# Kernel tuning notes

Measured on AMD Instinct MI355X. Metric: run time of the kernel, lower is better.

Reference implementation:

```python
import jax, jax.numpy as jnp
import numpy as np

HIDDEN = 2048
HEADS = 16
HEAD_DIM = HIDDEN // HEADS


def setup_inputs() -> dict:
    key = jax.random.key(0)
    ks = jax.random.split(key, 9)
    s = 0.02
    return {
        "hidden_state": jax.random.normal(ks[0], (2, 2048, HIDDEN), dtype=jnp.float32),
        "Wq": jax.random.normal(ks[1], (HIDDEN, HIDDEN), dtype=jnp.float32) * s,
        "bq": jnp.zeros((HIDDEN,), dtype=jnp.float32),
        "Wk": jax.random.normal(ks[2], (HIDDEN, HIDDEN), dtype=jnp.float32) * s,
        "bk": jnp.zeros((HIDDEN,), dtype=jnp.float32),
        "Wv": jax.random.normal(ks[3], (HIDDEN, HIDDEN), dtype=jnp.float32) * s,
        "bv": jnp.zeros((HIDDEN,), dtype=jnp.float32),
        "Wo": jax.random.normal(ks[4], (HIDDEN, HIDDEN), dtype=jnp.float32) * s,
        "bo": jnp.zeros((HIDDEN,), dtype=jnp.float32),
    }


def _split_head(x):
    b, s, _ = x.shape
    return x.reshape(b, s, HEADS, HEAD_DIM).transpose(0, 2, 1, 3)  # [B,H,S,D]


def reference(hidden_state, Wq, bq, Wk, bk, Wv, bv, Wo, bo):
    scale = 1.0 / (HEAD_DIM ** 0.5)
    # nn.Linear: x @ W.T + b
    q = _split_head(hidden_state @ Wq.T + bq)
    k = _split_head(hidden_state @ Wk.T + bk)
    v = _split_head(hidden_state @ Wv.T + bv)
    scores = jnp.einsum("bhqd,bhkd->bhqk", q, k) * scale  # [B,H,S,S]
    probs = jax.nn.softmax(scores, axis=-1)
    # dropout treated as identity (eval mode)
    out = jnp.einsum("bhqk,bhkd->bhqd", probs, v)  # [B,H,S,D]
    b, h, s, d = out.shape
    out = out.transpose(0, 2, 1, 3).reshape(b, s, h * d)
    return out @ Wo.T + bo
```

## Files before the change

### kernel.cpp

```cpp
#include <hip/hip_runtime.h>
#include <hip/hip_bf16.h>


typedef __attribute__((ext_vector_type(8))) short bf16x8;
typedef __attribute__((ext_vector_type(4))) float f32x4;
typedef unsigned short ushort_t;

#define MFMA_16x16x32(a, b, c) __builtin_amdgcn_mfma_f32_16x16x32_bf16((a), (b), (c), 0, 0, 0)

__device__ __forceinline__ ushort_t f2bf(float f) {
  unsigned int u = __builtin_bit_cast(unsigned int, f);
  u += 0x7fffu + ((u >> 16) & 1u);
  return (ushort_t)(u >> 16);
}

__device__ __forceinline__ void gload_lds16(const void* g, void* lds) {
  __builtin_amdgcn_global_load_lds(
      (const __attribute__((address_space(1))) unsigned int*)g,
      (__attribute__((address_space(3))) unsigned int*)(unsigned int)(unsigned long long)lds,
      16, 0, 0);
}

__global__ __launch_bounds__(256) void f2bf_kernel(const float* __restrict__ in,
                                                   ushort_t* __restrict__ out, int n4) {
  int i = blockIdx.x * blockDim.x + threadIdx.x;
  const int stride = gridDim.x * blockDim.x;
  for (; i < n4; i += stride) {
    const float4 v = ((const float4*)in)[i];
    ushort4 o;
    o.x = f2bf(v.x); o.y = f2bf(v.y); o.z = f2bf(v.z); o.w = f2bf(v.w);
    ((ushort4*)out)[i] = o;
  }
}

template <int MODE>
__global__ __launch_bounds__(256) void gemm_bt_kernel(const ushort_t* __restrict__ A,
                                                      const ushort_t* __restrict__ B,
                                                      const float* __restrict__ bias,
                                                      void* __restrict__ Cout,
                                                      int M, int N, int K) {
  __shared__ __align__(16) char smem[16384];
  char* sA = smem;
  char* sB = smem + 8192;
  const int tid = threadIdx.x;
  const int wave = tid >> 6;
  const int lane = tid & 63;
  const int wr = wave >> 1, wc = wave & 1;
  const int brow = blockIdx.y * 128;
  const int bcol = blockIdx.x * 128;

  const f32x4 fzero = {0.f, 0.f, 0.f, 0.f};
  f32x4 acc[4][4];
#pragma unroll
  for (int i = 0; i < 4; ++i)
#pragma unroll
    for (int j = 0; j < 4; ++j) acc[i][j] = fzero;

  const int srow = lane >> 2;
  const int koff = (lane & 3) * 8;

  for (int kt = 0; kt < K; kt += 32) {
#pragma unroll
    for (int c = 0; c < 2; ++c) {
      const int ch = wave + c * 4;
      gload_lds16(A + (size_t)(brow + ch * 16 + srow) * K + kt + koff, sA + ch * 1024);
      gload_lds16(B + (size_t)(bcol + ch * 16 + srow) * K + kt + koff, sB + ch * 1024);
    }
    __syncthreads();
    bf16x8 af[4], bfr[4];
#pragma unroll
    for (int i = 0; i < 4; ++i)
      af[i] = *(const bf16x8*)(sA + (wr * 64 + i * 16 + (lane & 15)) * 64 + (lane >> 4) * 16);
#pragma unroll
    for (int j = 0; j < 4; ++j)
      bfr[j] = *(const bf16x8*)(sB + (wc * 64 + j * 16 + (lane & 15)) * 64 + (lane >> 4) * 16);
#pragma unroll
    for (int i = 0; i < 4; ++i)
#pragma unroll
      for (int j = 0; j < 4; ++j) acc[i][j] = MFMA_16x16x32(af[i], bfr[j], acc[i][j]);
    __syncthreads();
  }

#pragma unroll
  for (int i = 0; i < 4; ++i) {
#pragma unroll
    for (int j = 0; j < 4; ++j) {
#pragma unroll
      for (int r = 0; r < 4; ++r) {
        const int row = brow + wr * 64 + i * 16 + (lane >> 4) * 4 + r;
        const int col = bcol + wc * 64 + j * 16 + (lane & 15);
        const float v = acc[i][j][r] + ((MODE == 2) ? bias[row] : bias[col]);
        if (MODE == 0) {
          ((float*)Cout)[(size_t)row * N + col] = v;
        } else if (MODE == 1) {
          const int b = row >> 11, s = row & 2047;
          const int h = col >> 7, d = col & 127;
          ((ushort_t*)Cout)[(((size_t)b * 16 + h) * 2048 + s) * 128 + d] = f2bf(v);
        } else {
          const int h = row >> 7, d = row & 127;
          const int b = col >> 11, s = col & 2047;
          ((ushort_t*)Cout)[(((size_t)b * 16 + h) * 128 + d) * 2048 + s] = f2bf(v);
        }
      }
    }
  }
}

__global__ __launch_bounds__(256) void attn_kernel(const ushort_t* __restrict__ Q,
                                                   const ushort_t* __restrict__ K,
                                                   const ushort_t* __restrict__ Vt,
                                                   ushort_t* __restrict__ O) {
  constexpr int S = 2048, D = 128, H = 16;
  __shared__ __align__(16) char smem[16384 + 16384 + 9216];
  char* sK = smem;
  char* sVt = smem + 16384;
  char* sP = smem + 32768;

  const int tid = threadIdx.x;
  const int wave = tid >> 6;
  const int lane = tid & 63;
  const int g = lane >> 4;
  const int l15 = lane & 15;
  const int qt = blockIdx.x & 31;
  const int bh = blockIdx.x >> 5;
  const int b = bh >> 4, h = bh & 15;

  const ushort_t* Qb = Q + (size_t)bh * S * D;
  const char* Kb = (const char*)(K + (size_t)bh * S * D);
  const char* Vtb = (const char*)(Vt + (size_t)bh * D * S);
  const int q0 = qt * 64 + wave * 16;

  bf16x8 aq[4];
  {
    const ushort_t* qrow = Qb + (size_t)(q0 + l15) * D + g * 8;
#pragma unroll
    for (int kk = 0; kk < 4; ++kk) aq[kk] = *(const bf16x8*)(qrow + kk * 32);
  }

  const char* kg[4];
  const char* vg[4];
#pragma unroll
  for (int i = 0; i < 4; ++i) {
    const int po = (wave * 4 + i) * 1024 + lane * 16;
    const int lk = po ^ (((po >> 8) & 7) << 4);
    kg[i] = Kb + (size_t)(lk >> 8) * 256 + (lk & 255);
    const int lv = po ^ (((po >> 7) & 7) << 4);
    vg[i] = Vtb + (size_t)(lv >> 7) * 4096 + (lv & 127);
  }

  const f32x4 fzero = {0.f, 0.f, 0.f, 0.f};
  f32x4 o[8];
#pragma unroll
  for (int nt = 0; nt < 8; ++nt) o[nt] = fzero;
  float row_m[4] = {-1e30f, -1e30f, -1e30f, -1e30f};
  float row_l[4] = {0.f, 0.f, 0.f, 0.f};

  char* sPw = sP + wave * 2304;
  const float scale = 0.08838834764831845f;
  const float LOG2E = 1.4426950408889634f;

  for (int kv0 = 0; kv0 < S; kv0 += 64) {
    __syncthreads();
#pragma unroll
    for (int i = 0; i < 4; ++i)
      gload_lds16(kg[i] + (size_t)kv0 * 256, sK + (wave * 4 + i) * 1024);
#pragma unroll
    for (int i = 0; i < 4; ++i)
      gload_lds16(vg[i] + (size_t)kv0 * 2, sVt + (wave * 4 + i) * 1024);
    __syncthreads();

    f32x4 sfrag[4];
#pragma unroll
    for (int nt = 0; nt < 4; ++nt) {
      sfrag[nt] = fzero;
#pragma unroll
      for (int kk = 0; kk < 4; ++kk) {
        const int row = nt * 16 + l15;
        const int la = row * 256 + kk * 64 + g * 16;
        const bf16x8 bk = *(const bf16x8*)(sK + (la ^ ((row & 7) << 4)));
        sfrag[nt] = MFMA_16x16x32(aq[kk], bk, sfrag[nt]);
      }
    }

#pragma unroll
    for (int r = 0; r < 4; ++r) {
      const float s0 = sfrag[0][r] * scale;
      const float s1 = sfrag[1][r] * scale;
      const float s2 = sfrag[2][r] * scale;
      const float s3 = sfrag[3][r] * scale;
      float mx = fmaxf(fmaxf(s0, s1), fmaxf(s2, s3));
      mx = fmaxf(mx, __shfl_xor(mx, 1));
      mx = fmaxf(mx, __shfl_xor(mx, 2));
      mx = fmaxf(mx, __shfl_xor(mx, 4));
      mx = fmaxf(mx, __shfl_xor(mx, 8));
      if (!__all(mx - row_m[r] <= 8.0f)) {
        const float nm = fmaxf(row_m[r], mx);
        const float corr = exp2f((row_m[r] - nm) * LOG2E);
        row_l[r] *= corr;
#pragma unroll
        for (int nt = 0; nt < 8; ++nt) o[nt][r] *= corr;
        row_m[r] = nm;
      }
      const float nm = row_m[r];
      const float p0 = exp2f((s0 - nm) * LOG2E);
      const float p1 = exp2f((s1 - nm) * LOG2E);
      const float p2 = exp2f((s2 - nm) * LOG2E);
      const float p3 = exp2f((s3 - nm) * LOG2E);
      float rs = (p0 + p1) + (p2 + p3);
      rs += __shfl_xor(rs, 1);
      rs += __shfl_xor(rs, 2);
      rs += __shfl_xor(rs, 4);
      rs += __shfl_xor(rs, 8);
      row_l[r] += rs;
      ushort_t* pr = (ushort_t*)(sPw + (g * 4 + r) * 144);
      pr[l15] = f2bf(p0);
      pr[16 + l15] = f2bf(p1);
      pr[32 + l15] = f2bf(p2);
      pr[48 + l15] = f2bf(p3);
    }

    const bf16x8 pa0 = *(const bf16x8*)(sPw + l15 * 144 + g * 16);
    const bf16x8 pa1 = *(const bf16x8*)(sPw + l15 * 144 + 64 + g * 16);
#pragma unroll
    for (int nt = 0; nt < 8; ++nt) {
      const int d = nt * 16 + l15;
      const int la0 = d * 128 + g * 16;
      const bf16x8 bv0 = *(const bf16x8*)(sVt + (la0 ^ ((d & 7) << 4)));
      o[nt] = MFMA_16x16x32(pa0, bv0, o[nt]);
      const bf16x8 bv1 = *(const bf16x8*)(sVt + ((la0 + 64) ^ ((d & 7) << 4)));
      o[nt] = MFMA_16x16x32(pa1, bv1, o[nt]);
    }
  }

#pragma unroll
  for (int r = 0; r < 4; ++r) {
    const float inv = 1.0f / row_l[r];
    const int srow = q0 + g * 4 + r;
    ushort_t* orow = O + ((size_t)b * S + srow) * (H * D) + h * D;
#pragma unroll
    for (int nt = 0; nt < 8; ++nt) orow[nt * 16 + l15] = f2bf(o[nt][r] * inv);
  }
}

extern "C" void kernel_launch(void* const* d_in, const int* in_sizes, int n_in,
                              void* d_out, int out_size, void* d_ws, size_t ws_size,
                              hipStream_t stream) {
  const float* hidden = (const float*)d_in[0];
  const float* Wq = (const float*)d_in[1];
  const float* bq = (const float*)d_in[2];
  const float* Wk = (const float*)d_in[3];
  const float* bk = (const float*)d_in[4];
  const float* Wv = (const float*)d_in[5];
  const float* bv = (const float*)d_in[6];
  const float* Wo = (const float*)d_in[7];
  const float* bo = (const float*)d_in[8];

  constexpr int M = 4096, N = 2048, Kd = 2048;
  char* ws = (char*)d_ws;
  ushort_t* hb  = (ushort_t*)(ws);
  ushort_t* wqb = (ushort_t*)(ws + (16u << 20));
  ushort_t* wkb = (ushort_t*)(ws + (16u << 20) + 1u * (8u << 20));
  ushort_t* wvb = (ushort_t*)(ws + (16u << 20) + 2u * (8u << 20));
  ushort_t* wob = (ushort_t*)(ws + (16u << 20) + 3u * (8u << 20));
  ushort_t* Qs  = (ushort_t*)(ws + (16u << 20) + 4u * (8u << 20));
  ushort_t* Ks  = Qs + (size_t)M * N;
  ushort_t* Vts = Ks + (size_t)M * N;
  ushort_t* AO  = Vts + (size_t)M * N;

  f2bf_kernel<<<2048, 256, 0, stream>>>(hidden, hb, M * Kd / 4);
  f2bf_kernel<<<1024, 256, 0, stream>>>(Wq, wqb, N * Kd / 4);
  f2bf_kernel<<<1024, 256, 0, stream>>>(Wk, wkb, N * Kd / 4);
  f2bf_kernel<<<1024, 256, 0, stream>>>(Wv, wvb, N * Kd / 4);
  f2bf_kernel<<<1024, 256, 0, stream>>>(Wo, wob, N * Kd / 4);

  dim3 gg(N / 128, M / 128);
  gemm_bt_kernel<1><<<gg, 256, 0, stream>>>(hb, wqb, bq, Qs, M, N, Kd);
  gemm_bt_kernel<1><<<gg, 256, 0, stream>>>(hb, wkb, bk, Ks, M, N, Kd);
  dim3 ggv(M / 128, N / 128);
  gemm_bt_kernel<2><<<ggv, 256, 0, stream>>>(wvb, hb, bv, Vts, N, M, Kd);
  attn_kernel<<<1024, 256, 0, stream>>>(Qs, Ks, Vts, AO);
  gemm_bt_kernel<0><<<gg, 256, 0, stream>>>(AO, wob, bo, d_out, M, N, Kd);
}
```

Measured before the change: 571.9 us.

## Fuse Q/K/V projections into one pipelined 256x256-tile GEMM kernel

Concatenates the bf16 Wq/Wk/Wv weights into one contiguous matrix and replaces three separate 128x128 GEMM launches with a single fused QKV kernel. The new kernel uses 512 threads, 256x256 tiles, a triple-buffered LDS pipeline fed by direct global-to-LDS loads, XOR-swizzled LDS addressing, block-index swizzling for L2 locality, and raised scheduling priority around the MFMA blocks. V is now computed as hidden x Wv^T and written transposed in the epilogue. The aim is to cut launch count, reuse each loaded A tile across more output columns, and hide memory latency. In exchange it uses 96KB of dynamic LDS and many accumulators, which limits occupancy, and the transposed V store is strided.

```diff
diff --git a/kernel.cpp b/kernel.cpp
--- a/kernel.cpp
+++ b/kernel.cpp
@@ -33,11 +33,135 @@
   }
 }
 
-template <int MODE>
+__global__ __launch_bounds__(512) void qkv_fused_kernel(
+    const ushort_t* __restrict__ A,
+    const ushort_t* __restrict__ W,
+    const float* __restrict__ bq, const float* __restrict__ bk,
+    const float* __restrict__ bv,
+    ushort_t* __restrict__ Qs, ushort_t* __restrict__ Ks,
+    ushort_t* __restrict__ Vts) {
+  constexpr int K = 2048, NT = K / 32;
+  extern __shared__ char sm[];
+  const int tid = threadIdx.x;
+  const int wave = tid >> 6, lane = tid & 63;
+  const int g = lane >> 4, l15 = lane & 15;
+  const int wr = wave >> 2, wc = wave & 3;
+
+  const int bid = blockIdx.x;
+  const int sw = (bid & 7) * 48 + (bid >> 3);
+  const int bx = sw % 24, by = sw / 24;
+  const int brow = by * 256, bcol = bx * 256;
+
+  const ushort_t* srcA[2];
+  const ushort_t* srcB[2];
+#pragma unroll
+  for (int j = 0; j < 2; ++j) {
+    const int p = (wave * 2 + j) * 64 + lane;
+    const int row = p >> 2;
+    const int col = (p & 3) ^ ((row >> 1) & 3);
+    srcA[j] = A + (size_t)(brow + row) * K + col * 8;
+    srcB[j] = W + (size_t)(bcol + row) * K + col * 8;
+  }
+
+  const int fph = (l15 >> 1) & 3;
+  const int aOff = (wr * 128 + l15) * 64 + ((g ^ fph) << 4);
+  const int bOff = (wc * 64 + l15) * 64 + ((g ^ fph) << 4) + 16384;
+
+  char* p0 = sm;
+  char* p1 = sm + 32768;
+  char* p2 = sm + 65536;
+
+#define STAGE_A(P, t)                                                        \
+  {                                                                          \
+    gload_lds16(srcA[0] + (t) * 32, (P) + (wave * 2 + 0) * 1024);            \
+    gload_lds16(srcA[1] + (t) * 32, (P) + (wave * 2 + 1) * 1024);            \
+  }
+#define STAGE_B(P, t)                                                        \
+  {                                                                          \
+    gload_lds16(srcB[0] + (t) * 32, (P) + 16384 + (wave * 2 + 0) * 1024);    \
+    gload_lds16(srcB[1] + (t) * 32, (P) + 16384 + (wave * 2 + 1) * 1024);    \
+  }
+
+  const f32x4 fzero = {0.f, 0.f, 0.f, 0.f};
+  f32x4 acc[8][4];
+#pragma unroll
+  for (int i = 0; i < 8; ++i)
+#pragma unroll
+    for (int j = 0; j < 4; ++j) acc[i][j] = fzero;
+
+  STAGE_A(p0, 0); STAGE_B(p0, 0);
+  STAGE_A(p1, 1); STAGE_B(p1, 1);
+  asm volatile("s_waitcnt vmcnt(4)" ::: "memory");
+  __builtin_amdgcn_sched_barrier(0);
+  __builtin_amdgcn_s_barrier();
+  __builtin_amdgcn_sched_barrier(0);
+
+  for (int kt = 0; kt < NT; ++kt) {
+    const bool doStage = (kt < NT - 2);
+    if (doStage) STAGE_A(p2, kt + 2);
+    bf16x8 bfr[4], afr[4];
+#pragma unroll
+    for (int j = 0; j < 4; ++j) bfr[j] = *(const bf16x8*)(p0 + bOff + j * 1024);
+#pragma unroll
+    for (int i = 0; i < 4; ++i) afr[i] = *(const bf16x8*)(p0 + aOff + i * 1024);
+    __builtin_amdgcn_s_setprio(1);
+#pragma unroll
+    for (int i = 0; i < 4; ++i)
+#pragma unroll
+      for (int j = 0; j < 4; ++j) acc[i][j] = MFMA_16x16x32(afr[i], bfr[j], acc[i][j]);
+    __builtin_amdgcn_s_setprio(0);
+    if (doStage) STAGE_B(p2, kt + 2);
+#pragma unroll
+    for (int i = 0; i < 4; ++i) afr[i] = *(const bf16x8*)(p0 + aOff + (4 + i) * 1024);
+    __builtin_amdgcn_s_setprio(1);
+#pragma unroll
+    for (int i = 0; i < 4; ++i)
+#pragma unroll
+      for (int j = 0; j < 4; ++j) acc[4 + i][j] = MFMA_16x16x32(afr[i], bfr[j], acc[4 + i][j]);
+    __builtin_amdgcn_s_setprio(0);
+    if (doStage) {
+      asm volatile("s_waitcnt vmcnt(4) lgkmcnt(0)" ::: "memory");
+    } else {
+      asm volatile("s_waitcnt vmcnt(0) lgkmcnt(0)" ::: "memory");
+    }
+    __builtin_amdgcn_sched_barrier(0);
+    __builtin_amdgcn_s_barrier();
+    __builtin_amdgcn_sched_barrier(0);
+    char* t = p0; p0 = p1; p1 = p2; p2 = t;
+  }
+#undef STAGE_A
+#undef STAGE_B
+
+  const int seg = bcol >> 11;
+  const float* bias = (seg == 0) ? bq : ((seg == 1) ? bk : bv);
+#pragma unroll
+  for (int j = 0; j < 4; ++j) {
+    const int gcol = bcol + wc * 64 + j * 16 + l15;
+    const int n = gcol & 2047;
+    const float bb = bias[n];
+    const int h = n >> 7, d = n & 127;
+#pragma unroll
+    for (int i = 0; i < 8; ++i) {
+#pragma unroll
+      for (int r = 0; r < 4; ++r) {
+        const int grow = brow + wr * 128 + i * 16 + g * 4 + r;
+        const int b_ = grow >> 11, s_ = grow & 2047;
+        const float v = acc[i][j][r] + bb;
+        if (seg == 0)
+          Qs[(((size_t)b_ * 16 + h) * 2048 + s_) * 128 + d] = f2bf(v);
+        else if (seg == 1)
+          Ks[(((size_t)b_ * 16 + h) * 2048 + s_) * 128 + d] = f2bf(v);
+        else
+          Vts[(((size_t)b_ * 16 + h) * 128 + d) * 2048 + s_] = f2bf(v);
+      }
+    }
+  }
+}
+
 __global__ __launch_bounds__(256) void gemm_bt_kernel(const ushort_t* __restrict__ A,
                                                       const ushort_t* __restrict__ B,
                                                       const float* __restrict__ bias,
-                                                      void* __restrict__ Cout,
+                                                      float* __restrict__ Cout,
                                                       int M, int N, int K) {
   __shared__ __align__(16) char smem[16384];
   char* sA = smem;
@@ -82,28 +206,15 @@
   }
 
 #pragma unroll
-  for (int i = 0; i < 4; ++i) {
-#pragma unroll
-    for (int j = 0; j < 4; ++j) {
+  for (int i = 0; i < 4; ++i)
+#pragma unroll
+    for (int j = 0; j < 4; ++j)
 #pragma unroll
       for (int r = 0; r < 4; ++r) {
         const int row = brow + wr * 64 + i * 16 + (lane >> 4) * 4 + r;
         const int col = bcol + wc * 64 + j * 16 + (lane & 15);
-        const float v = acc[i][j][r] + ((MODE == 2) ? bias[row] : bias[col]);
-        if (MODE == 0) {
-          ((float*)Cout)[(size_t)row * N + col] = v;
-        } else if (MODE == 1) {
-          const int b = row >> 11, s = row & 2047;
-          const int h = col >> 7, d = col & 127;
-          ((ushort_t*)Cout)[(((size_t)b * 16 + h) * 2048 + s) * 128 + d] = f2bf(v);
-        } else {
-          const int h = row >> 7, d = row & 127;
-          const int b = col >> 11, s = col & 2047;
-          ((ushort_t*)Cout)[(((size_t)b * 16 + h) * 128 + d) * 2048 + s] = f2bf(v);
-        }
+        Cout[(size_t)row * N + col] = acc[i][j][r] + bias[col];
       }
-    }
-  }
 }
 
 __global__ __launch_bounds__(256) void attn_kernel(const ushort_t* __restrict__ Q,
@@ -257,27 +368,22 @@
 
   constexpr int M = 4096, N = 2048, Kd = 2048;
   char* ws = (char*)d_ws;
-  ushort_t* hb  = (ushort_t*)(ws);
-  ushort_t* wqb = (ushort_t*)(ws + (16u << 20));
-  ushort_t* wkb = (ushort_t*)(ws + (16u << 20) + 1u * (8u << 20));
-  ushort_t* wvb = (ushort_t*)(ws + (16u << 20) + 2u * (8u << 20));
-  ushort_t* wob = (ushort_t*)(ws + (16u << 20) + 3u * (8u << 20));
-  ushort_t* Qs  = (ushort_t*)(ws + (16u << 20) + 4u * (8u << 20));
-  ushort_t* Ks  = Qs + (size_t)M * N;
-  ushort_t* Vts = Ks + (size_t)M * N;
-  ushort_t* AO  = Vts + (size_t)M * N;
+  ushort_t* hb   = (ushort_t*)(ws);
+  ushort_t* wqkv = (ushort_t*)(ws + (16u << 20));
+  ushort_t* wob  = (ushort_t*)(ws + (40u << 20));
+  ushort_t* Qs   = (ushort_t*)(ws + (48u << 20));
+  ushort_t* Ks   = Qs + (size_t)M * N;
+  ushort_t* Vts  = Ks + (size_t)M * N;
+  ushort_t* AO   = Vts + (size_t)M * N;
 
   f2bf_kernel<<<2048, 256, 0, stream>>>(hidden, hb, M * Kd / 4);
-  f2bf_kernel<<<1024, 256, 0, stream>>>(Wq, wqb, N * Kd / 4);
-  f2bf_kernel<<<1024, 256, 0, stream>>>(Wk, wkb, N * Kd / 4);
-  f2bf_kernel<<<1024, 256, 0, stream>>>(Wv, wvb, N * Kd / 4);
+  f2bf_kernel<<<1024, 256, 0, stream>>>(Wq, wqkv, N * Kd / 4);
+  f2bf_kernel<<<1024, 256, 0, stream>>>(Wk, wqkv + (size_t)N * Kd, N * Kd / 4);
+  f2bf_kernel<<<1024, 256, 0, stream>>>(Wv, wqkv + 2 * (size_t)N * Kd, N * Kd / 4);
   f2bf_kernel<<<1024, 256, 0, stream>>>(Wo, wob, N * Kd / 4);
 
+  qkv_fused_kernel<<<384, 512, 98304, stream>>>(hb, wqkv, bq, bk, bv, Qs, Ks, Vts);
+  attn_kernel<<<1024, 256, 0, stream>>>(Qs, Ks, Vts, AO);
   dim3 gg(N / 128, M / 128);
-  gemm_bt_kernel<1><<<gg, 256, 0, stream>>>(hb, wqb, bq, Qs, M, N, Kd);
-  gemm_bt_kernel<1><<<gg, 256, 0, stream>>>(hb, wkb, bk, Ks, M, N, Kd);
-  dim3 ggv(M / 128, N / 128);
-  gemm_bt_kernel<2><<<ggv, 256, 0, stream>>>(wvb, hb, bv, Vts, N, M, Kd);
-  attn_kernel<<<1024, 256, 0, stream>>>(Qs, Ks, Vts, AO);
-  gemm_bt_kernel<0><<<gg, 256, 0, stream>>>(AO, wob, bo, d_out, M, N, Kd);
-}
+  gemm_bt_kernel<<<gg, 256, 0, stream>>>(AO, wob, bo, (float*)d_out, M, N, Kd);
+}
```

After: 559.6 us. 2.2% less time.
